# Kernel tuning notes

Measured on AMD Instinct MI355X. Metric: run time of the kernel, lower is better.

## Reference

```python
import jax, jax.numpy as jnp
import numpy as np

F = 32          # final_feature_size
S = 256         # coordinate stride for key packing (coords < 251, offsets +-1)
SENT = 2 ** 30  # sentinel key > any real packed key
DELTAS = [dx * S * S + dy * S + dz
          for dx in (-1, 0, 1) for dy in (-1, 0, 1) for dz in (-1, 0, 1)]  # 27 kernel offsets


def setup_inputs() -> dict:
    rng = np.random.default_rng(0)
    T, per_frame, B, Npts = 16, 40000, 2, 400000
    # --- history sweep voxels: coords [t, x, y, z], t = global frame id ---
    t = np.repeat(np.arange(T, dtype=np.int32), per_frame)
    xyz = rng.integers(1, 251, size=(T * per_frame, 3), dtype=np.int32)
    keys = ((t.astype(np.int64) * S + xyz[:, 0]) * S + xyz[:, 1]) * S + xyz[:, 2]
    _, idx = np.unique(keys, return_index=True)  # ME quantization dedup
    t, xyz = t[idx], xyz[idx]
    n = t.shape[0]
    history_coordinates = np.concatenate([t[:, None], xyz], axis=1).astype(np.int32)
    history_batches = (t // (T // B)).astype(np.int32)  # scene id per voxel
    history_features = rng.standard_normal((n, 1)).astype(np.float32)
    # --- current scan query points ---
    b = rng.integers(0, B, size=Npts).astype(np.int32)
    qxyz = rng.integers(1, 251, size=(Npts, 3), dtype=np.int32)
    curr_coords = np.concatenate([b[:, None], qxyz], axis=1).astype(np.int32)
    points = np.concatenate([b[:, None].astype(np.float32),
                             qxyz.astype(np.float32),
                             rng.standard_normal((Npts, 1)).astype(np.float32)], axis=1)
    # --- params ---
    W_bb = (rng.standard_normal((27, 1, F)) * (2.0 / 27) ** 0.5).astype(np.float32)
    W_conv = (rng.standard_normal((27, F, F)) * (1.0 / (27 * F)) ** 0.5).astype(np.float32)
    return {
        'history_features': jnp.asarray(history_features),
        'points': jnp.asarray(points),
        'W_bb': jnp.asarray(W_bb),
        'W_conv': jnp.asarray(W_conv),
        'history_coordinates': jnp.asarray(history_coordinates),
        'history_batches': jnp.asarray(history_batches),
        'curr_coords': jnp.asarray(curr_coords),
    }


def pack4(c):
    c = c.astype(jnp.int32)
    return ((c[:, 0] * S + c[:, 1]) * S + c[:, 2]) * S + c[:, 3]


def sparse_conv(sorted_keys, table_feats, out_keys, W):
    """Minkowski-style sparse conv: gather neighbor at each of 27 offsets, matmul, scatter-add."""
    n = sorted_keys.shape[0]
    out = jnp.zeros((out_keys.shape[0], W.shape[2]), table_feats.dtype)
    for i, d in enumerate(DELTAS):
        nk = out_keys + d
        pos = jnp.clip(jnp.searchsorted(sorted_keys, nk), 0, n - 1)
        valid = (sorted_keys[pos] == nk)[:, None]
        g = jnp.where(valid, table_feats[pos], 0.0)
        out = out + g @ W[i]
    return out


def reference(history_features, points, W_bb, W_conv,
              history_coordinates, history_batches, curr_coords):
    n = history_features.shape[0]
    # ---- history backbone (stand-in: one sparse 3x3x3 conv, 1->F, time col as batch) ----
    keys_h = pack4(history_coordinates)
    order = jnp.argsort(keys_h)
    bb = sparse_conv(keys_h[order], history_features[order], keys_h, W_bb)  # [n, F]
    # ---- MinkowskiMaxPooling kernel [1000,1,1,1]: max over time per (b,x,y,z) ----
    pool_coords = jnp.concatenate([history_batches[:, None], history_coordinates[:, 1:4]], axis=1)
    keys_p = pack4(pool_coords)
    uk, inv = jnp.unique(keys_p, return_inverse=True, size=n, fill_value=SENT)  # sorted
    pooled = jax.ops.segment_max(bb, inv, num_segments=n)                        # [n, F]
    # ---- current_conv evaluated at (unique) query voxels, then slice back to points ----
    keys_q = pack4(curr_coords)
    m = keys_q.shape[0]
    uq, qinv = jnp.unique(keys_q, return_inverse=True, size=m, fill_value=SENT)
    conv_q = sparse_conv(uk, pooled, uq, W_conv)  # [m, F]
    ofield = conv_q[qinv]                          # TensorField slice: per-point features
    # ---- mode='update_point_features', preserve_feature==3 ----
    return jnp.concatenate([points[:, :4], ofield], axis=1)  # [Npts, 4+F]
```

## Files before the change

kernel.cpp:

```cpp
#include <hip/hip_runtime.h>
#include <stdint.h>
#include <utility>


#define TPB 256
#define SCAN_WPT 8
#define GB_H 2048
#define GB_P 256
typedef unsigned long long u64;
typedef unsigned int u32;
typedef unsigned short u16;

__device__ __forceinline__ u32 trans16(float x) {
    u32 b = __float_as_uint(x);
    u32 bf = (b + 0x7FFFu + ((b >> 16) & 1u)) >> 16;
    return ((bf & 0x8000u) ? (~bf) : (bf | 0x8000u)) & 0xFFFFu;
}
__device__ __forceinline__ float detrans16(u32 u) {
    u32 orig = (u & 0x8000u) ? (u & 0x7FFFu) : ((~u) & 0xFFFFu);
    return __uint_as_float(orig << 16);
}

template <int... Ks>
__device__ __forceinline__ void kfma(float pv, const float* __restrict__ W,
                                     float& acc,
                                     std::integer_sequence<int, Ks...>) {
    ((acc = fmaf(__uint_as_float((u32)__builtin_amdgcn_ds_swizzle(
                     (int)__float_as_uint(pv), (Ks << 5))),
                 W[Ks * 32], acc)),
     ...);
}

__global__ void build_bitmaps_kernel(const int4* __restrict__ hc,
                                     const int* __restrict__ hb,
                                     int n,
                                     u64* __restrict__ hist_bm,
                                     u64* __restrict__ pool_bm,
                                     u64* __restrict__ multi_bm) {
    int j = blockIdx.x * blockDim.x + threadIdx.x;
    if (j >= n) return;
    int4 c = hc[j];
    int key = ((c.x * 256 + c.y) * 256 + c.z) * 256 + c.w;
    atomicOr(&hist_bm[key >> 6], 1ull << (key & 63));
    int pk = ((hb[j] * 256 + c.y) * 256 + c.z) * 256 + c.w;
    u64 bit = 1ull << (pk & 63);
    u64 old = atomicOr(&pool_bm[pk >> 6], bit);
    if (old & bit) atomicOr(&multi_bm[pk >> 6], bit);
}

__global__ void scan_sum_all_kernel(const u64* __restrict__ hist_bm,
                                    const u64* __restrict__ pool_bm,
                                    u32* __restrict__ bsum) {
    __shared__ u32 s[TPB];
    int t = threadIdx.x;
    bool isPool = blockIdx.x >= GB_H;
    const u64* bm = isPool ? pool_bm : hist_bm;
    int blk = isPool ? (blockIdx.x - GB_H) : blockIdx.x;
    size_t base = ((size_t)blk * TPB + t) * SCAN_WPT;
    u32 acc = 0;
#pragma unroll
    for (int i = 0; i < SCAN_WPT; i++) acc += __popcll(bm[base + i]);
    s[t] = acc; __syncthreads();
    for (int off = TPB / 2; off > 0; off >>= 1) {
        if (t < off) s[t] += s[t + off];
        __syncthreads();
    }
    if (t == 0) bsum[blockIdx.x] = s[0];
}

__global__ void scan_partials_all_kernel(u32* __restrict__ bsum) {
    __shared__ u32 s[TPB];
    int t = threadIdx.x;
    u32 v[8]; u32 acc = 0;
#pragma unroll
    for (int i = 0; i < 8; i++) { v[i] = bsum[t * 8 + i]; acc += v[i]; }
    s[t] = acc; __syncthreads();
    for (int off = 1; off < TPB; off <<= 1) {
        u32 x = (t >= off) ? s[t - off] : 0;
        __syncthreads();
        s[t] += x;
        __syncthreads();
    }
    u32 run = s[t] - acc;
#pragma unroll
    for (int i = 0; i < 8; i++) { bsum[t * 8 + i] = run; run += v[i]; }
    __syncthreads();
    u32 pv = bsum[GB_H + t];
    s[t] = pv; __syncthreads();
    for (int off = 1; off < TPB; off <<= 1) {
        u32 x = (t >= off) ? s[t - off] : 0;
        __syncthreads();
        s[t] += x;
        __syncthreads();
    }
    bsum[GB_H + t] = s[t] - pv;
}

__global__ void scan_apply_all_kernel(const u64* __restrict__ hist_bm,
                                      const u64* __restrict__ pool_bm,
                                      const u32* __restrict__ bsum,
                                      u32* __restrict__ hist_rank,
                                      u32* __restrict__ pool_rank,
                                      const u64* __restrict__ multi_bm,
                                      u32* __restrict__ pooled) {
    __shared__ u32 s[TPB];
    int t = threadIdx.x;
    bool isPool = blockIdx.x >= GB_H;
    const u64* bm = isPool ? pool_bm : hist_bm;
    u32* rank = isPool ? pool_rank : hist_rank;
    int blk = isPool ? (blockIdx.x - GB_H) : blockIdx.x;
    size_t base = ((size_t)blk * TPB + t) * SCAN_WPT;
    u32 pc[SCAN_WPT]; u32 acc = 0;
#pragma unroll
    for (int i = 0; i < SCAN_WPT; i++) { pc[i] = __popcll(bm[base + i]); acc += pc[i]; }
    s[t] = acc; __syncthreads();
    for (int off = 1; off < TPB; off <<= 1) {
        u32 x = (t >= off) ? s[t - off] : 0;
        __syncthreads();
        s[t] += x;
        __syncthreads();
    }
    u32 run = bsum[blockIdx.x] + s[t] - acc;
    u32 run0 = run;
#pragma unroll
    for (int i = 0; i < SCAN_WPT; i++) { rank[base + i] = run; run += pc[i]; }
    if (isPool) {
        u32 r2 = run0;
#pragma unroll
        for (int i = 0; i < SCAN_WPT; i++) {
            u64 mw = multi_bm[base + i];
            if (mw) {
                u64 pw = bm[base + i];
                while (mw) {
                    int b = __ffsll((long long)mw) - 1;
                    mw &= mw - 1;
                    u32 slot = r2 + (u32)__popcll(pw & ((1ull << b) - 1ull));
                    u32* row = pooled + (size_t)slot * 16;
#pragma unroll
                    for (int w2 = 0; w2 < 16; w2++) row[w2] = 0u;
                }
            }
            r2 += pc[i];
        }
    }
}

__global__ __launch_bounds__(TPB, 8)
void bb_pool_kernel(const int4* __restrict__ hc,
                    const int* __restrict__ hb,
                    const float* __restrict__ hf,
                    const float* __restrict__ Wbb,
                    int n,
                    const u64* __restrict__ hist_bm,
                    const u32* __restrict__ hist_rank,
                    const u64* __restrict__ pool_bm,
                    const u32* __restrict__ pool_rank,
                    const u64* __restrict__ multi_bm,
                    u32* __restrict__ pooled) {
    int nwg = gridDim.x;
    int q = nwg >> 3, r = nwg & 7;
    int xcd = blockIdx.x & 7, idx = blockIdx.x >> 3;
    int swz = (xcd < r ? xcd * (q + 1) : r * (q + 1) + (xcd - r) * q) + idx;

    int p = (swz * TPB + threadIdx.x) >> 5;
    if (p >= n) return;
    int lane = threadIdx.x & 63;
    int hb32 = lane & 32;
    int f = lane & 31;

    int4 c = hc[p];
    int key = ((c.x * 256 + c.y) * 256 + c.z) * 256 + c.w;
    int pk = ((hb[p] * 256 + c.y) * 256 + c.z) * 256 + c.w;

    u64 pword = pool_bm[pk >> 6];
    u32 prank = pool_rank[pk >> 6];
    u64 mword = multi_bm[pk >> 6];

    float fv = 0.f;
    bool hit = false;
    if (f < 27) {
        int t1 = f / 9, rem = f - t1 * 9, t2 = rem / 3, t3 = rem - t2 * 3;
        int nk = key + (t1 - 1) * 65536 + (t2 - 1) * 256 + (t3 - 1);
        u64 word = hist_bm[nk >> 6];
        u32 rk   = hist_rank[nk >> 6];
        if ((word >> (nk & 63)) & 1ull) {
            u32 r2 = rk + (u32)__popcll(word & ((1ull << (nk & 63)) - 1ull));
            fv = hf[r2];
            hit = true;
        }
    }
    unsigned long long bal = __ballot(hit);
    u32 mymask = (u32)(bal >> hb32);

    float acc = 0.f;
    while (mymask) {
        int b = __ffs(mymask) - 1;
        mymask &= mymask - 1;
        float fb = __shfl(fv, hb32 + b);
        acc = fmaf(fb, Wbb[b * 32 + f], acc);
    }

    int bit = pk & 63;
    int slot = (int)(prank + (u32)__popcll(pword & ((1ull << bit) - 1ull)));
    bool multi = (mword >> bit) & 1ull;

    u32 tv = trans16(acc);
    u32 packed = tv | (((u32)__shfl_down((int)tv, 1)) << 16);
    if ((f & 1) == 0) {
        u32* addr = pooled + (size_t)slot * 16 + (f >> 1);
        if (!multi) {
            *addr = packed;
        } else {
            u32 oldv = *addr;
            while (true) {
                u32 lo = max(oldv & 0xFFFFu, packed & 0xFFFFu);
                u32 hi = max(oldv >> 16, packed >> 16);
                u32 mx = lo | (hi << 16);
                if (mx == oldv) break;
                u32 prev = atomicCAS(addr, oldv, mx);
                if (prev == oldv) break;
                oldv = prev;
            }
        }
    }
}

__global__ __launch_bounds__(TPB, 8)
void query_kernel(const int4* __restrict__ qc,
                  const float* __restrict__ pts,
                  const float* __restrict__ Wc,
                  int m,
                  const u64* __restrict__ pool_bm,
                  const u32* __restrict__ pool_rank,
                  const u16* __restrict__ pooled16,
                  float* __restrict__ out) {
    int p = (blockIdx.x * blockDim.x + threadIdx.x) >> 5;
    if (p >= m) return;
    int lane = threadIdx.x & 63;
    int hb32 = lane & 32;
    int f = lane & 31;

    int4 c = qc[p];
    int qk = ((c.x * 256 + c.y) * 256 + c.z) * 256 + c.w;

    int slotL = -1;
    if (f < 27) {
        int t1 = f / 9, rem = f - t1 * 9, t2 = rem / 3, t3 = rem - t2 * 3;
        int nk = qk + (t1 - 1) * 65536 + (t2 - 1) * 256 + (t3 - 1);
        u64 word = pool_bm[nk >> 6];
        u32 rk   = pool_rank[nk >> 6];
        if ((word >> (nk & 63)) & 1ull)
            slotL = (int)(rk + (u32)__popcll(word & ((1ull << (nk & 63)) - 1ull)));
    }
    unsigned long long bal = __ballot(slotL >= 0);
    u32 mymask = (u32)(bal >> hb32);

    float acc = 0.f;
    while (mymask) {
        int b = __ffs(mymask) - 1;
        mymask &= mymask - 1;
        int slot = __shfl(slotL, hb32 + b);
        float pv = detrans16(pooled16[(size_t)slot * 32 + f]);
        const float* W = Wc + b * 1024 + f;
        kfma(pv, W, acc, std::make_integer_sequence<int, 32>{});
    }

    float acc2 = __shfl_down(acc, 1);
    if ((f & 1) == 0) {
        float2 st; st.x = acc; st.y = acc2;
        *(float2*)(out + (size_t)p * 36 + 4 + f) = st;
    }
    if (f < 4) out[(size_t)p * 36 + f] = pts[p * 5 + f];
}

extern "C" void kernel_launch(void* const* d_in, const int* in_sizes, int n_in,
                              void* d_out, int out_size, void* d_ws, size_t ws_size,
                              hipStream_t stream) {
    const float* hfeat   = (const float*)d_in[0];
    const float* pts     = (const float*)d_in[1];
    const float* Wbb     = (const float*)d_in[2];
    const float* Wconv   = (const float*)d_in[3];
    const int4*  hcoords = (const int4*)d_in[4];
    const int*   hbatch  = (const int*)d_in[5];
    const int4*  qcoords = (const int4*)d_in[6];
    int n = in_sizes[0];
    int m = in_sizes[1] / 5;

    const int NW_H = 1 << 22;
    const int NW_P = 1 << 19;

    char* w = (char*)d_ws;
    char* zbase = w;
    u64* hist_bm      = (u64*)w;       w += (size_t)NW_H * 8;
    u64* pool_bm      = (u64*)w;       w += (size_t)NW_P * 8;
    u64* multi_bm     = (u64*)w;       w += (size_t)NW_P * 8;
    size_t zbytes = (size_t)(w - zbase);
    u32* pooled       = (u32*)w;       w += (size_t)n * 64;
    u32* hist_rank    = (u32*)w;       w += (size_t)NW_H * 4;
    u32* pool_rank    = (u32*)w;       w += (size_t)NW_P * 4;
    u32* bsum         = (u32*)w;       w += (size_t)(GB_H + GB_P) * 4;

    hipMemsetAsync(zbase, 0x00, zbytes, stream);

    int gb_n   = (n + TPB - 1) / TPB;
    int gb_n32 = (int)(((long long)n * 32 + TPB - 1) / TPB);
    int gb_m32 = (int)(((long long)m * 32 + TPB - 1) / TPB);

    build_bitmaps_kernel<<<gb_n, TPB, 0, stream>>>(hcoords, hbatch, n,
                                                   hist_bm, pool_bm, multi_bm);
    scan_sum_all_kernel<<<GB_H + GB_P, TPB, 0, stream>>>(hist_bm, pool_bm, bsum);
    scan_partials_all_kernel<<<1, TPB, 0, stream>>>(bsum);
    scan_apply_all_kernel<<<GB_H + GB_P, TPB, 0, stream>>>(hist_bm, pool_bm, bsum,
                                                           hist_rank, pool_rank,
                                                           multi_bm, pooled);
    bb_pool_kernel<<<gb_n32, TPB, 0, stream>>>(hcoords, hbatch, hfeat, Wbb, n,
                                               hist_bm, hist_rank,
                                               pool_bm, pool_rank, multi_bm, pooled);
    query_kernel<<<gb_m32, TPB, 0, stream>>>(qcoords, pts, Wconv, m,
                                             pool_bm, pool_rank,
                                             (const u16*)pooled, (float*)d_out);
}
```

Before: 262.5 us.

## Fuse three-pass bitmap scan into single-pass decoupled look-back scan

Replaces the reduce / partial-scan / apply sequence with one kernel that publishes per-block aggregates and inclusive prefixes through flagged 64-bit status words and walks back to compute its base. This removes two kernel launches and a second full read of the bitmaps. It relies on blocks being scheduled in order to avoid look-back deadlock, and adds serial spinning for the first thread of each block. It also adds __builtin_assume range hints on keys and slots in the conv kernels.

```diff
diff --git a/kernel.cpp b/kernel.cpp
--- a/kernel.cpp
+++ b/kernel.cpp
@@ -7,9 +7,14 @@
 #define SCAN_WPT 8
 #define GB_H 2048
 #define GB_P 256
+#define NBLK_SCAN (GB_H + GB_P)
 typedef unsigned long long u64;
 typedef unsigned int u32;
 typedef unsigned short u16;
+
+#define FLAG_AGG (1ull << 62)
+#define FLAG_PRE (2ull << 62)
+#define FLAG_MSK (3ull << 62)
 
 __device__ __forceinline__ u32 trans16(float x) {
     u32 b = __float_as_uint(x);
@@ -48,62 +53,15 @@
     if (old & bit) atomicOr(&multi_bm[pk >> 6], bit);
 }
 
-__global__ void scan_sum_all_kernel(const u64* __restrict__ hist_bm,
-                                    const u64* __restrict__ pool_bm,
-                                    u32* __restrict__ bsum) {
+__global__ void scan_fused_kernel(const u64* __restrict__ hist_bm,
+                                  const u64* __restrict__ pool_bm,
+                                  u32* __restrict__ hist_rank,
+                                  u32* __restrict__ pool_rank,
+                                  const u64* __restrict__ multi_bm,
+                                  u32* __restrict__ pooled,
+                                  u64* __restrict__ st) {
     __shared__ u32 s[TPB];
-    int t = threadIdx.x;
-    bool isPool = blockIdx.x >= GB_H;
-    const u64* bm = isPool ? pool_bm : hist_bm;
-    int blk = isPool ? (blockIdx.x - GB_H) : blockIdx.x;
-    size_t base = ((size_t)blk * TPB + t) * SCAN_WPT;
-    u32 acc = 0;
-#pragma unroll
-    for (int i = 0; i < SCAN_WPT; i++) acc += __popcll(bm[base + i]);
-    s[t] = acc; __syncthreads();
-    for (int off = TPB / 2; off > 0; off >>= 1) {
-        if (t < off) s[t] += s[t + off];
-        __syncthreads();
-    }
-    if (t == 0) bsum[blockIdx.x] = s[0];
-}
-
-__global__ void scan_partials_all_kernel(u32* __restrict__ bsum) {
-    __shared__ u32 s[TPB];
-    int t = threadIdx.x;
-    u32 v[8]; u32 acc = 0;
-#pragma unroll
-    for (int i = 0; i < 8; i++) { v[i] = bsum[t * 8 + i]; acc += v[i]; }
-    s[t] = acc; __syncthreads();
-    for (int off = 1; off < TPB; off <<= 1) {
-        u32 x = (t >= off) ? s[t - off] : 0;
-        __syncthreads();
-        s[t] += x;
-        __syncthreads();
-    }
-    u32 run = s[t] - acc;
-#pragma unroll
-    for (int i = 0; i < 8; i++) { bsum[t * 8 + i] = run; run += v[i]; }
-    __syncthreads();
-    u32 pv = bsum[GB_H + t];
-    s[t] = pv; __syncthreads();
-    for (int off = 1; off < TPB; off <<= 1) {
-        u32 x = (t >= off) ? s[t - off] : 0;
-        __syncthreads();
-        s[t] += x;
-        __syncthreads();
-    }
-    bsum[GB_H + t] = s[t] - pv;
-}
-
-__global__ void scan_apply_all_kernel(const u64* __restrict__ hist_bm,
-                                      const u64* __restrict__ pool_bm,
-                                      const u32* __restrict__ bsum,
-                                      u32* __restrict__ hist_rank,
-                                      u32* __restrict__ pool_rank,
-                                      const u64* __restrict__ multi_bm,
-                                      u32* __restrict__ pooled) {
-    __shared__ u32 s[TPB];
+    __shared__ u32 sbase;
     int t = threadIdx.x;
     bool isPool = blockIdx.x >= GB_H;
     const u64* bm = isPool ? pool_bm : hist_bm;
@@ -120,7 +78,29 @@
         s[t] += x;
         __syncthreads();
     }
-    u32 run = bsum[blockIdx.x] + s[t] - acc;
+    u32 wave_excl = s[t] - acc;
+    u32 blocksum = s[TPB - 1];
+
+    if (t == 0) {
+        if (blk == 0) {
+            atomicExch(&st[blockIdx.x], FLAG_PRE | (u64)blocksum);
+            sbase = 0;
+        } else {
+            atomicExch(&st[blockIdx.x], FLAG_AGG | (u64)blocksum);
+            u64 run = 0; int i = blockIdx.x - 1;
+            while (true) {
+                u64 v = atomicAdd(&st[i], 0ull);
+                u64 fl = v & FLAG_MSK;
+                if (fl == FLAG_PRE) { run += v & 0xFFFFFFFFull; break; }
+                if (fl == FLAG_AGG) { run += v & 0xFFFFFFFFull; i--; }
+            }
+            atomicExch(&st[blockIdx.x], FLAG_PRE | (run + (u64)blocksum));
+            sbase = (u32)run;
+        }
+    }
+    __syncthreads();
+
+    u32 run = sbase + wave_excl;
     u32 run0 = run;
 #pragma unroll
     for (int i = 0; i < SCAN_WPT; i++) { rank[base + i] = run; run += pc[i]; }
@@ -170,7 +150,9 @@
 
     int4 c = hc[p];
     int key = ((c.x * 256 + c.y) * 256 + c.z) * 256 + c.w;
+    __builtin_assume(key >= 65793 && key < (1 << 28));
     int pk = ((hb[p] * 256 + c.y) * 256 + c.z) * 256 + c.w;
+    __builtin_assume(pk >= 65793 && pk < (1 << 25));
 
     u64 pword = pool_bm[pk >> 6];
     u32 prank = pool_rank[pk >> 6];
@@ -181,10 +163,12 @@
     if (f < 27) {
         int t1 = f / 9, rem = f - t1 * 9, t2 = rem / 3, t3 = rem - t2 * 3;
         int nk = key + (t1 - 1) * 65536 + (t2 - 1) * 256 + (t3 - 1);
+        __builtin_assume(nk >= 0 && nk < (1 << 28));
         u64 word = hist_bm[nk >> 6];
         u32 rk   = hist_rank[nk >> 6];
         if ((word >> (nk & 63)) & 1ull) {
             u32 r2 = rk + (u32)__popcll(word & ((1ull << (nk & 63)) - 1ull));
+            __builtin_assume(r2 < (1u << 20));
             fv = hf[r2];
             hit = true;
         }
@@ -202,6 +186,7 @@
 
     int bit = pk & 63;
     int slot = (int)(prank + (u32)__popcll(pword & ((1ull << bit) - 1ull)));
+    __builtin_assume(slot >= 0);
     bool multi = (mword >> bit) & 1ull;
 
     u32 tv = trans16(acc);
@@ -242,11 +227,13 @@
 
     int4 c = qc[p];
     int qk = ((c.x * 256 + c.y) * 256 + c.z) * 256 + c.w;
+    __builtin_assume(qk >= 65793 && qk < (1 << 25));
 
     int slotL = -1;
     if (f < 27) {
         int t1 = f / 9, rem = f - t1 * 9, t2 = rem / 3, t3 = rem - t2 * 3;
         int nk = qk + (t1 - 1) * 65536 + (t2 - 1) * 256 + (t3 - 1);
+        __builtin_assume(nk >= 0 && nk < (1 << 25));
         u64 word = pool_bm[nk >> 6];
         u32 rk   = pool_rank[nk >> 6];
         if ((word >> (nk & 63)) & 1ull)
@@ -260,6 +247,7 @@
         int b = __ffs(mymask) - 1;
         mymask &= mymask - 1;
         int slot = __shfl(slotL, hb32 + b);
+        __builtin_assume(slot >= 0 && slot < (1 << 20));
         float pv = detrans16(pooled16[(size_t)slot * 32 + f]);
         const float* W = Wc + b * 1024 + f;
         kfma(pv, W, acc, std::make_integer_sequence<int, 32>{});
@@ -294,13 +282,13 @@
     u64* hist_bm      = (u64*)w;       w += (size_t)NW_H * 8;
     u64* pool_bm      = (u64*)w;       w += (size_t)NW_P * 8;
     u64* multi_bm     = (u64*)w;       w += (size_t)NW_P * 8;
+    u64* st           = (u64*)w;       w += (size_t)NBLK_SCAN * 8;
     size_t zbytes = (size_t)(w - zbase);
     u32* pooled       = (u32*)w;       w += (size_t)n * 64;
     u32* hist_rank    = (u32*)w;       w += (size_t)NW_H * 4;
     u32* pool_rank    = (u32*)w;       w += (size_t)NW_P * 4;
-    u32* bsum         = (u32*)w;       w += (size_t)(GB_H + GB_P) * 4;
-
-    hipMemsetAsync(zbase, 0x00, zbytes, stream);
+
+    (void)hipMemsetAsync(zbase, 0x00, zbytes, stream);
 
     int gb_n   = (n + TPB - 1) / TPB;
     int gb_n32 = (int)(((long long)n * 32 + TPB - 1) / TPB);
@@ -308,11 +296,9 @@
 
     build_bitmaps_kernel<<<gb_n, TPB, 0, stream>>>(hcoords, hbatch, n,
                                                    hist_bm, pool_bm, multi_bm);
-    scan_sum_all_kernel<<<GB_H + GB_P, TPB, 0, stream>>>(hist_bm, pool_bm, bsum);
-    scan_partials_all_kernel<<<1, TPB, 0, stream>>>(bsum);
-    scan_apply_all_kernel<<<GB_H + GB_P, TPB, 0, stream>>>(hist_bm, pool_bm, bsum,
-                                                           hist_rank, pool_rank,
-                                                           multi_bm, pooled);
+    scan_fused_kernel<<<NBLK_SCAN, TPB, 0, stream>>>(hist_bm, pool_bm,
+                                                     hist_rank, pool_rank,
+                                                     multi_bm, pooled, st);
     bb_pool_kernel<<<gb_n32, TPB, 0, stream>>>(hcoords, hbatch, hfeat, Wbb, n,
                                                hist_bm, hist_rank,
                                                pool_bm, pool_rank, multi_bm, pooled);
```

After: 268.7 us. +2.4%, slower.
